# Kernel tuning notes

Measured on AMD Instinct MI355X. Metric: run time of the kernel, lower is better.

The kernel has to match this reference:

```python
import jax, jax.numpy as jnp
import numpy as np

N, E, HID, ED, L, H, D = 65536, 262144, 256, 64, 2, 8, 32
FF = 4 * HID
A_START = 8192  # first action gripper node; nodes [A_START:] are the T*K action nodes


def _ln(x, s, b, eps=1e-5):
    mu = jnp.mean(x, -1, keepdims=True)
    var = jnp.var(x, -1, keepdims=True)
    return (x - mu) * jax.lax.rsqrt(var + eps) * s + b


def _gnn_forward(x, edge_attr, edge_index, Wq, Wk, Wv, WeK, WeV, Wo,
                 ln1_s, ln1_b, ffn_w1, ffn_b1, ffn_w2, ffn_b2, ln2_s, ln2_b):
    # Hetero graph transformer over the single ('gripper','action','gripper') relation:
    # per-layer edge-indexed gather -> multi-head attention with edge features ->
    # segment softmax over incoming edges -> scatter-aggregate -> residual/LN/FFN.
    n = x.shape[0]
    e = edge_attr.shape[0]
    src, dst = edge_index[0], edge_index[1]
    inv_sqrt_d = np.float32(1.0 / np.sqrt(D))
    for l in range(Wq.shape[0]):
        q = (x @ Wq[l]).reshape(n, H, D)
        k = (x @ Wk[l]).reshape(n, H, D)
        v = (x @ Wv[l]).reshape(n, H, D)
        kj = k[src] + (edge_attr @ WeK[l]).reshape(e, H, D)  # [E,H,D] gathered keys + edge bias
        vj = v[src] + (edge_attr @ WeV[l]).reshape(e, H, D)
        score = jnp.einsum('ehd,ehd->eh', q[dst], kj) * inv_sqrt_d  # [E,H]
        smax = jax.ops.segment_max(score, dst, num_segments=n)
        p = jnp.exp(score - smax[dst])
        denom = jax.ops.segment_sum(p, dst, num_segments=n)
        alpha = p / denom[dst]  # segment softmax over incoming edges
        agg = jax.ops.segment_sum((alpha[..., None] * vj).reshape(e, H * D), dst, num_segments=n)
        x = _ln(x + agg @ Wo[l], ln1_s[l], ln1_b[l])
        hid = jax.nn.gelu(x @ ffn_w1[l] + ffn_b1[l], approximate=False) @ ffn_w2[l] + ffn_b2[l]
        x = _ln(x + hid, ln2_s[l], ln2_b[l])
    return x


def setup_inputs() -> dict:
    key = jax.random.key(0)
    ks = iter(jax.random.split(key, 16))
    w = lambda shape: jax.random.normal(next(ks), shape, jnp.float32) * 0.05
    return {
        "all_gripper_feats": jax.random.normal(next(ks), (N, HID), jnp.float32),
        "edge_attr": jax.random.normal(next(ks), (E, ED), jnp.float32),
        "Wq": w((L, HID, H * D)), "Wk": w((L, HID, H * D)), "Wv": w((L, HID, H * D)),
        "WeK": w((L, ED, H * D)), "WeV": w((L, ED, H * D)), "Wo": w((L, H * D, HID)),
        "ln1_s": jnp.ones((L, HID), jnp.float32), "ln1_b": jnp.zeros((L, HID), jnp.float32),
        "ffn_w1": w((L, HID, FF)), "ffn_b1": jnp.zeros((L, FF), jnp.float32),
        "ffn_w2": w((L, FF, HID)), "ffn_b2": jnp.zeros((L, HID), jnp.float32),
        "ln2_s": jnp.ones((L, HID), jnp.float32), "ln2_b": jnp.zeros((L, HID), jnp.float32),
        "head_w1": w((HID, HID)), "head_b1": jnp.zeros((HID,), jnp.float32),
        "head_w2": w((HID, 7)), "head_b2": jnp.zeros((7,), jnp.float32),
        "edge_index": jax.random.randint(next(ks), (2, E), 0, N),
        "action_start": A_START,
    }


def reference(all_gripper_feats, edge_attr, Wq, Wk, Wv, WeK, WeV, Wo,
              ln1_s, ln1_b, ffn_w1, ffn_b1, ffn_w2, ffn_b2, ln2_s, ln2_b,
              head_w1, head_b1, head_w2, head_b2, edge_index, action_start):
    x = _gnn_forward(all_gripper_feats, edge_attr, edge_index, Wq, Wk, Wv, WeK, WeV, Wo,
                     ln1_s, ln1_b, ffn_w1, ffn_b1, ffn_w2, ffn_b2, ln2_s, ln2_b)
    a = x[action_start:]  # action gripper nodes (T*K, hidden)
    return jax.nn.gelu(a @ head_w1 + head_b1, approximate=False) @ head_w2 + head_b2  # (T*K, 7)
```

## Files before the change

kernel.cpp:

```cpp
#include <hip/hip_runtime.h>
#include <hip/hip_bf16.h>
#include <math.h>

#define NN     65536
#define NE     262144
#define HIDN   256
#define EDIM   64
#define NHEAD  8
#define FFN    1024
#define ASTART 8192
#define NACT   (NN - ASTART)
#define NCH    32768
#define NCHP   (NCH + 128)
#define NCHUNK (NE / NCH)
#define DPC    (NN / NCHUNK)
#define RCH    32768

typedef __attribute__((ext_vector_type(8))) short short8;
typedef __attribute__((ext_vector_type(4))) short short4v;
typedef __attribute__((ext_vector_type(4))) float float4v;
typedef __hip_bfloat16 bf16;

__device__ __forceinline__ float b2f(short s) {
    union { unsigned u; float f; } c;
    c.u = ((unsigned)(unsigned short)s) << 16;
    return c.f;
}
__device__ __forceinline__ short f2b(float f) {
    __hip_bfloat16 h = __float2bfloat16(f);
    return *reinterpret_cast<short*>(&h);
}
__device__ __forceinline__ float gelu_fast(float v) {
    const float x  = v * 0.70710678118654752f;
    const float ax = fabsf(x);
    const float t  = __builtin_amdgcn_rcpf(1.0f + 0.3275911f * ax);
    const float y  = t * (0.254829592f + t * (-0.284496736f + t * (1.421413741f +
                     t * (-1.453152027f + t * 1.061405429f))));
    const float e  = __expf(-x * x);
    float erf = 1.0f - y * e;
    erf = copysignf(erf, x);
    return 0.5f * v * (1.0f + erf);
}
__device__ __forceinline__ void gload16(const void* g, void* l) {
    __builtin_amdgcn_global_load_lds(
        (const __attribute__((address_space(1))) void*)(uintptr_t)g,
        (__attribute__((address_space(3))) void*)(unsigned)(uintptr_t)l,
        16, 0, 0);
}

__global__ void convert_kernel(const float* __restrict__ src,
                               bf16* __restrict__ dst, int n) {
    int i = blockIdx.x * 256 + threadIdx.x;
    if (i < n) dst[i] = __float2bfloat16(src[i]);
}
__global__ void convert4_kernel(const float* __restrict__ src,
                                bf16* __restrict__ dst, int n4) {
    int i = blockIdx.x * 256 + threadIdx.x;
    if (i >= n4) return;
    float4v f = *(const float4v*)(src + (size_t)i * 4);
    short4v o;
    #pragma unroll
    for (int j = 0; j < 4; ++j) o[j] = f2b(f[j]);
    *(short4v*)((short*)dst + (size_t)i * 4) = o;
}

__global__ void gather_kernel(const float* __restrict__ src,
                              const int* __restrict__ perm,
                              bf16* __restrict__ dst) {
    int i = blockIdx.x * 256 + threadIdx.x;
    if (i >= NE * 16) return;
    const int p = i >> 4, j = i & 15;
    const float4v f = *(const float4v*)(src + (size_t)perm[p] * EDIM + j * 4);
    short4v o;
    #pragma unroll
    for (int k = 0; k < 4; ++k) o[k] = f2b(f[k]);
    *(short4v*)((short*)dst + (size_t)p * EDIM + j * 4) = o;
}

__global__ void transpose_kernel(const float* __restrict__ src,
                                 bf16* __restrict__ dst, int R, int Cc) {
    int idx = blockIdx.x * 256 + threadIdx.x;
    if (idx >= R * Cc) return;
    int r = idx / Cc, c = idx - r * Cc;
    dst[(size_t)c * R + r] = __float2bfloat16(src[idx]);
}

__global__ void hist_kernel(const int* __restrict__ dstI, int* __restrict__ cnt) {
    int i = blockIdx.x * 256 + threadIdx.x;
    if (i < NE) atomicAdd(&cnt[dstI[i]], 1);
}
__global__ void scan1_kernel(const int* __restrict__ cnt, int* __restrict__ rp,
                             int* __restrict__ bsum) {
    __shared__ int s[256];
    int t = threadIdx.x, i = blockIdx.x * 256 + t;
    int v = cnt[i]; s[t] = v; __syncthreads();
    for (int off = 1; off < 256; off <<= 1) {
        int x = (t >= off) ? s[t - off] : 0; __syncthreads();
        s[t] += x; __syncthreads();
    }
    rp[i] = s[t] - v;
    if (t == 255) bsum[blockIdx.x] = s[255];
}
__global__ void scan2_kernel(int* __restrict__ bsum) {
    __shared__ int s[256];
    int t = threadIdx.x; int v = bsum[t]; s[t] = v; __syncthreads();
    for (int off = 1; off < 256; off <<= 1) {
        int x = (t >= off) ? s[t - off] : 0; __syncthreads();
        s[t] += x; __syncthreads();
    }
    bsum[t] = s[t] - v;
}
__global__ void scan3_kernel(int* __restrict__ rp, const int* __restrict__ bsum,
                             int* __restrict__ cursor) {
    int i = blockIdx.x * 256 + threadIdx.x;
    int v = rp[i] + bsum[i >> 8];
    rp[i] = v; cursor[i] = v;
    if (i == 0) rp[NN] = NE;
}
__global__ void scatter_kernel(const int* __restrict__ srcI, const int* __restrict__ dstI,
                               int* __restrict__ cursor, int* __restrict__ perm,
                               int* __restrict__ src_s, int* __restrict__ dst_s) {
    int e = blockIdx.x * 256 + threadIdx.x;
    if (e >= NE) return;
    int d = dstI[e];
    int pos = atomicAdd(&cursor[d], 1);
    perm[pos] = e; src_s[pos] = srcI[e]; dst_s[pos] = d;
}

template<int AMODE, bool DO_GELU>
__global__ __launch_bounds__(256) void gemm_kernel(
    const void* __restrict__ A,
    const bf16* __restrict__ BT,
    const bf16* __restrict__ bias,
    bf16* __restrict__ C,
    int M, int Nn, int K,
    const int* __restrict__ perm, int permN)
{
    __shared__ __align__(16) short Ls[4][128 * 32];

    const int gx   = gridDim.x;
    const int nwg  = gx * gridDim.y;
    const int orig = blockIdx.y * gx + blockIdx.x;
    const int q8   = nwg >> 3, r8 = nwg & 7;
    const int xcd  = orig & 7, rk = orig >> 3;
    const int nid  = (xcd < r8 ? xcd * (q8 + 1) : r8 * (q8 + 1) + (xcd - r8) * q8) + rk;
    const int by   = nid / gx;
    const int bx   = nid - by * gx;

    const int t    = threadIdx.x;
    const int wave = t >> 6;
    const int lane = t & 63;
    const int l15  = lane & 15;
    const int quad = lane >> 4;
    const int wm   = (wave & 1) * 64;
    const int wn   = (wave >> 1) * 64;
    const int bm   = by * 128;
    const int bn   = bx * 128;
    const int srow = t >> 2;
    const int sw   = srow & 3;
    const int scolB = ((t & 3) ^ sw) * 8;
    const int scolA = (t & 3) * 8;

    const short* Ab = (const short*)A  + (size_t)(bm + srow) * K + scolB;
    const short* Bb = (const short*)BT + (size_t)(bn + srow) * K + scolB;
    const float* Af0 = nullptr;
    const float* Af1 = nullptr;
    if (AMODE == 1) {
        Af0 = (const float*)A + (size_t)(bm + srow) * K + scolA;
        Af1 = Af0 + (size_t)64 * K;
    } else if (AMODE == 2) {
        int i0 = bm + srow;       if (i0 >= permN) i0 = permN - 1;
        int i1 = bm + 64 + srow;  if (i1 >= permN) i1 = permN - 1;
        const int pr0 = perm[i0];
        const int pr1 = perm[i1];
        Af0 = (const float*)A + (size_t)pr0 * K + scolA;
        Af1 = (const float*)A + (size_t)pr1 * K + scolA;
    }
    const int offW  = wave * 1024;
    const int offTs = (t * 16) ^ (sw << 4);
    const int qs16  = (quad ^ (l15 & 3)) * 16;

    float4v acc[4][4];
    #pragma unroll
    for (int i = 0; i < 4; ++i)
        #pragma unroll
        for (int j = 0; j < 4; ++j) acc[i][j] = (float4v){0.f, 0.f, 0.f, 0.f};

    const int nt = K >> 5;

    auto STAGE = [&](int b, int k0) {
        char* lA = (char*)Ls[b];
        char* lB = (char*)Ls[2 + b];
        if (AMODE == 0) {
            gload16(Ab + k0,                  lA + offW);
            gload16(Ab + (size_t)64 * K + k0, lA + 4096 + offW);
        } else {
            #pragma unroll
            for (int i = 0; i < 2; ++i) {
                const float* s = (i ? Af1 : Af0) + k0;
                float4v f0 = *(const float4v*)s;
                float4v f1 = *(const float4v*)(s + 4);
                short8 w;
                #pragma unroll
                for (int j = 0; j < 4; ++j) { w[j] = f2b(f0[j]); w[4 + j] = f2b(f1[j]); }
                *(short8*)(lA + i * 4096 + offTs) = w;
            }
        }
        gload16(Bb + k0,                  lB + offW);
        gload16(Bb + (size_t)64 * K + k0, lB + 4096 + offW);
    };

    STAGE(0, 0);
    __syncthreads();

    for (int kt = 0; kt < nt; ++kt) {
        const int cur = kt & 1;
        if (kt + 1 < nt) STAGE(cur ^ 1, (kt + 1) * 32);

        const char* lA = (const char*)Ls[cur];
        const char* lB = (const char*)Ls[2 + cur];
        short8 afr[4], bfr[4];
        #pragma unroll
        for (int i = 0; i < 4; ++i)
            afr[i] = *(const short8*)(lA + (wm + i * 16 + l15) * 64 + qs16);
        #pragma unroll
        for (int j = 0; j < 4; ++j)
            bfr[j] = *(const short8*)(lB + (wn + j * 16 + l15) * 64 + qs16);
        #pragma unroll
        for (int i = 0; i < 4; ++i)
            #pragma unroll
            for (int j = 0; j < 4; ++j)
                acc[i][j] = __builtin_amdgcn_mfma_f32_16x16x32_bf16(afr[i], bfr[j], acc[i][j], 0, 0, 0);
        __syncthreads();
    }

    short* Ct = (short*)Ls;
    #pragma unroll
    for (int j = 0; j < 4; ++j) {
        const int col  = wn + j * 16 + l15;
        const int pc   = col ^ (quad << 4);
        const float bv = bias ? b2f(((const short*)bias)[bn + col]) : 0.0f;
        #pragma unroll
        for (int i = 0; i < 4; ++i) {
            const int row0 = wm + i * 16 + quad * 4;
            #pragma unroll
            for (int r = 0; r < 4; ++r) {
                float v = acc[i][j][r] + bv;
                if (DO_GELU) v = gelu_fast(v);
                Ct[(row0 + r) * 128 + pc] = f2b(v);
            }
        }
    }
    __syncthreads();
    #pragma unroll
    for (int it = 0; it < 8; ++it) {
        const int row = wave * 32 + it + ((lane >> 4) << 3);
        const int cs  = (lane & 15) * 8;
        const int pcs = cs ^ (((row >> 2) & 3) << 4);
        short8 w = *(const short8*)&Ct[row * 128 + pcs];
        *(short8*)((short*)C + (size_t)(bm + row) * Nn + bn + cs) = w;
    }
}

__global__ __launch_bounds__(256) void score_kernel(
    const bf16* __restrict__ q, const bf16* __restrict__ k,
    const bf16* __restrict__ eK,
    const int* __restrict__ src_s, const int* __restrict__ dst_s,
    short* __restrict__ pbuf, int e0, int qkstride)
{
    const int p = e0 + blockIdx.x * 4 + (threadIdx.x >> 6);
    const int lane = threadIdx.x & 63;
    const int s = src_s[p], d = dst_s[p];
    const int off = lane * 4;

    const short4v qv = *(const short4v*)((const short*)q  + (size_t)d * qkstride + off);
    const short4v kv = *(const short4v*)((const short*)k  + (size_t)s * qkstride + off);
    const short4v ev = *(const short4v*)((const short*)eK + (size_t)(p - e0) * HIDN + off);
    float x = 0.f;
    #pragma unroll
    for (int j = 0; j < 4; ++j) x += b2f(qv[j]) * (b2f(kv[j]) + b2f(ev[j]));
    x += __shfl_xor(x, 1);
    x += __shfl_xor(x, 2);
    x += __shfl_xor(x, 4);
    if ((lane & 7) == 0) {
        const float sc = fminf(fmaxf(x * 0.17677669529663689f, -30.f), 30.f);
        pbuf[(size_t)p * NHEAD + (lane >> 3)] = f2b(expf(sc));
    }
}

__global__ __launch_bounds__(256) void agg_kernel(
    const short* __restrict__ pbuf, const bf16* __restrict__ v,
    const bf16* __restrict__ eV,
    const int* __restrict__ src_s, const int* __restrict__ rp,
    float* __restrict__ agg, int e0, int e1x, int dlo)
{
    const int d = dlo + blockIdx.x * 4 + (threadIdx.x >> 6);
    const int lane = threadIdx.x & 63;
    const int es = rp[d], ee = rp[d + 1];
    if (es < e0 || es >= e1x) return;
    const int h = lane >> 3, off = lane * 4;

    float a0 = 0.f, a1 = 0.f, a2 = 0.f, a3 = 0.f;
    if (es < ee) {
        float den = 0.f;
        for (int p = es; p < ee; ++p) den += b2f(pbuf[(size_t)p * NHEAD + h]);
        const float rden = 1.0f / den;
        for (int p = es; p < ee; ++p) {
            const float al = b2f(pbuf[(size_t)p * NHEAD + h]) * rden;
            const int s = src_s[p];
            const short4v vv = *(const short4v*)((const short*)v  + (size_t)s * HIDN + off);
            const short4v ev = *(const short4v*)((const short*)eV + (size_t)(p - e0) * HIDN + off);
            a0 += al * (b2f(vv[0]) + b2f(ev[0]));
            a1 += al * (b2f(vv[1]) + b2f(ev[1]));
            a2 += al * (b2f(vv[2]) + b2f(ev[2]));
            a3 += al * (b2f(vv[3]) + b2f(ev[3]));
        }
    }
    *(float4v*)(agg + (size_t)d * HIDN + off) = (float4v){a0, a1, a2, a3};
}

__global__ __launch_bounds__(256) void ln_kernel(
    bf16* __restrict__ x, const bf16* __restrict__ t,
    const bf16* __restrict__ sc, const bf16* __restrict__ bi, int r0)
{
    const int row = r0 + blockIdx.x * 4 + (threadIdx.x >> 6);
    const int lane = threadIdx.x & 63;
    const size_t base = (size_t)row * HIDN + lane * 4;
    const size_t tbase = (size_t)(row - r0) * HIDN + lane * 4;
    const short4v xv = *(const short4v*)((const short*)x + base);
    const short4v tv = *(const short4v*)((const short*)t + tbase);
    float v[4];
    #pragma unroll
    for (int j = 0; j < 4; ++j) v[j] = b2f(xv[j]) + b2f(tv[j]);
    float sum = v[0] + v[1] + v[2] + v[3];
    float ssq = v[0]*v[0] + v[1]*v[1] + v[2]*v[2] + v[3]*v[3];
    #pragma unroll
    for (int m = 1; m < 64; m <<= 1) { sum += __shfl_xor(sum, m); ssq += __shfl_xor(ssq, m); }
    const float mean = sum * (1.0f / 256.0f);
    const float var  = fmaxf(ssq * (1.0f / 256.0f) - mean * mean, 0.0f);
    const float rstd = rsqrtf(var + 1e-5f);
    const short4v sv = *(const short4v*)((const short*)sc + lane * 4);
    const short4v bv = *(const short4v*)((const short*)bi + lane * 4);
    short4v out;
    #pragma unroll
    for (int j = 0; j < 4; ++j)
        out[j] = f2b((v[j] - mean) * rstd * b2f(sv[j]) + b2f(bv[j]));
    *(short4v*)((short*)x + base) = out;
}

__global__ __launch_bounds__(256) void head2_kernel(
    const bf16* __restrict__ h1, const bf16* __restrict__ w2T,
    const bf16* __restrict__ b2, float* __restrict__ out)
{
    const int row = blockIdx.x * 4 + (threadIdx.x >> 6);
    const int lane = threadIdx.x & 63;
    const int off = lane * 4;
    const short4v hv = *(const short4v*)((const short*)h1 + (size_t)row * HIDN + off);
    float hf[4];
    #pragma unroll
    for (int j = 0; j < 4; ++j) hf[j] = b2f(hv[j]);
    float acc[7];
    #pragma unroll
    for (int jc = 0; jc < 7; ++jc) {
        const short4v wv = *(const short4v*)((const short*)w2T + jc * HIDN + off);
        float a = hf[0]*b2f(wv[0]) + hf[1]*b2f(wv[1]) + hf[2]*b2f(wv[2]) + hf[3]*b2f(wv[3]);
        #pragma unroll
        for (int m = 1; m < 64; m <<= 1) a += __shfl_xor(a, m);
        acc[jc] = a;
    }
    if (lane < 7) {
        float r = lane == 0 ? acc[0] : lane == 1 ? acc[1] : lane == 2 ? acc[2] :
                  lane == 3 ? acc[3] : lane == 4 ? acc[4] : lane == 5 ? acc[5] : acc[6];
        out[(size_t)row * 7 + lane] = r + b2f(((const short*)b2)[lane]);
    }
}

extern "C" void kernel_launch(void* const* d_in, const int* in_sizes, int n_in,
                              void* d_out, int out_size, void* d_ws, size_t ws_size,
                              hipStream_t stream)
{
    const float* xin   = (const float*)d_in[0];
    const float* eattr = (const float*)d_in[1];
    const float* Wq    = (const float*)d_in[2];
    const float* Wk    = (const float*)d_in[3];
    const float* Wv    = (const float*)d_in[4];
    const float* WeK   = (const float*)d_in[5];
    const float* WeV   = (const float*)d_in[6];
    const float* Wo    = (const float*)d_in[7];
    const float* ln1s  = (const float*)d_in[8];
    const float* ln1b  = (const float*)d_in[9];
    const float* fw1   = (const float*)d_in[10];
    const float* fb1   = (const float*)d_in[11];
    const float* fw2   = (const float*)d_in[12];
    const float* fb2   = (const float*)d_in[13];
    const float* ln2s  = (const float*)d_in[14];
    const float* ln2b  = (const float*)d_in[15];
    const float* hw1   = (const float*)d_in[16];
    const float* hb1   = (const float*)d_in[17];
    const float* hw2   = (const float*)d_in[18];
    const float* hb2   = (const float*)d_in[19];
    const int*  eidx   = (const int*)d_in[20];
    const int*  srcI   = eidx;
    const int*  dstI   = eidx + NE;

    char* base = (char*)d_ws;
    size_t off = 0;
    auto carve = [&](size_t bytes) -> char* {
        char* p = base + off;
        off += (bytes + 255) & ~(size_t)255;
        return p;
    };
    bf16*  x_b    = (bf16*) carve((size_t)NN * HIDN * 2);
    bf16*  qk_b   = (bf16*) carve((size_t)NN * 2 * HIDN * 2);
    bf16*  v_b    = (bf16*) carve((size_t)NN * HIDN * 2);
    bf16*  echunk = (bf16*) carve((size_t)NCHP * HIDN * 2);
    short* pbuf   = (short*)carve((size_t)NE * NHEAD * 2);
    int*   perm   = (int*)  carve((size_t)NE * 4);
    int*   src_s  = (int*)  carve((size_t)NE * 4);
    int*   dst_s  = (int*)  carve((size_t)NE * 4);
    int*   rowp   = (int*)  carve((size_t)(NN + 1) * 4);
    bf16*  WqkT   = (bf16*) carve((size_t)2 * HIDN * HIDN * 2);
    bf16*  WvT    = (bf16*) carve((size_t)HIDN * HIDN * 2);
    bf16*  WoT    = (bf16*) carve((size_t)HIDN * HIDN * 2);
    bf16*  WeKT   = (bf16*) carve((size_t)HIDN * EDIM * 2);
    bf16*  WeVT   = (bf16*) carve((size_t)HIDN * EDIM * 2);
    bf16*  W1T    = (bf16*) carve((size_t)FFN * HIDN * 2);
    bf16*  W2T    = (bf16*) carve((size_t)HIDN * FFN * 2);
    bf16*  HW1T   = (bf16*) carve((size_t)HIDN * HIDN * 2);
    bf16*  HW2T   = (bf16*) carve((size_t)8 * HIDN * 2);
    bf16*  c_ln1s = (bf16*) carve((size_t)2 * HIDN * 2);
    bf16*  c_ln1b = (bf16*) carve((size_t)2 * HIDN * 2);
    bf16*  c_ln2s = (bf16*) carve((size_t)2 * HIDN * 2);
    bf16*  c_ln2b = (bf16*) carve((size_t)2 * HIDN * 2);
    bf16*  c_fb1  = (bf16*) carve((size_t)2 * FFN * 2);
    bf16*  c_fb2  = (bf16*) carve((size_t)2 * HIDN * 2);
    bf16*  c_hb1  = (bf16*) carve((size_t)HIDN * 2);
    bf16*  c_hb2  = (bf16*) carve((size_t)16 * 2);
    const size_t off_mand = off;
    bf16*  eattr_s = (bf16*) carve((size_t)(NE + 128) * EDIM * 2);
    const bool eg = (off <= ws_size);
    if (off_mand > ws_size) return;

    int* cnt    = (int*)echunk;
    int* cursor = cnt + NN;
    int* bsum   = cursor + NN;
    float* agg    = (float*)qk_b;
    bf16*  tmp_b  = v_b;
    bf16*  hid    = qk_b;
    bf16*  ffnout = v_b;

    const int TB = 256;
    #define GRID1(n) dim3(((n) + TB - 1) / TB)

    convert4_kernel<<<GRID1(NN * HIDN / 4), TB, 0, stream>>>(xin, x_b, NN * HIDN / 4);
    convert_kernel<<<GRID1(2 * HIDN), TB, 0, stream>>>(ln1s, c_ln1s, 2 * HIDN);
    convert_kernel<<<GRID1(2 * HIDN), TB, 0, stream>>>(ln1b, c_ln1b, 2 * HIDN);
    convert_kernel<<<GRID1(2 * HIDN), TB, 0, stream>>>(ln2s, c_ln2s, 2 * HIDN);
    convert_kernel<<<GRID1(2 * HIDN), TB, 0, stream>>>(ln2b, c_ln2b, 2 * HIDN);
    convert_kernel<<<GRID1(2 * FFN), TB, 0, stream>>>(fb1, c_fb1, 2 * FFN);
    convert_kernel<<<GRID1(2 * HIDN), TB, 0, stream>>>(fb2, c_fb2, 2 * HIDN);
    convert_kernel<<<GRID1(HIDN), TB, 0, stream>>>(hb1, c_hb1, HIDN);
    convert_kernel<<<1, TB, 0, stream>>>(hb2, c_hb2, 7);
    transpose_kernel<<<GRID1(HIDN * HIDN), TB, 0, stream>>>(hw1, HW1T, HIDN, HIDN);
    transpose_kernel<<<GRID1(HIDN * 7), TB, 0, stream>>>(hw2, HW2T, HIDN, 7);

    hipMemsetAsync(cnt, 0, (size_t)NN * 4, stream);
    hist_kernel<<<GRID1(NE), TB, 0, stream>>>(dstI, cnt);
    scan1_kernel<<<NN / 256, 256, 0, stream>>>(cnt, rowp, bsum);
    scan2_kernel<<<1, 256, 0, stream>>>(bsum);
    scan3_kernel<<<NN / 256, 256, 0, stream>>>(rowp, bsum, cursor);
    scatter_kernel<<<GRID1(NE), TB, 0, stream>>>(srcI, dstI, cursor, perm, src_s, dst_s);
    if (eg) gather_kernel<<<GRID1(NE * 16), TB, 0, stream>>>(eattr, perm, eattr_s);

    for (int l = 0; l < 2; ++l) {
        transpose_kernel<<<GRID1(HIDN * HIDN), TB, 0, stream>>>(Wq + (size_t)l*HIDN*HIDN, WqkT, HIDN, HIDN);
        transpose_kernel<<<GRID1(HIDN * HIDN), TB, 0, stream>>>(Wk + (size_t)l*HIDN*HIDN, WqkT + (size_t)HIDN*HIDN, HIDN, HIDN);
        transpose_kernel<<<GRID1(HIDN * HIDN), TB, 0, stream>>>(Wv + (size_t)l*HIDN*HIDN, WvT, HIDN, HIDN);
        transpose_kernel<<<GRID1(EDIM * HIDN), TB, 0, stream>>>(WeK + (size_t)l*EDIM*HIDN, WeKT, EDIM, HIDN);
        transpose_kernel<<<GRID1(EDIM * HIDN), TB, 0, stream>>>(WeV + (size_t)l*EDIM*HIDN, WeVT, EDIM, HIDN);
        transpose_kernel<<<GRID1(HIDN * HIDN), TB, 0, stream>>>(Wo + (size_t)l*HIDN*HIDN, WoT, HIDN, HIDN);
        transpose_kernel<<<GRID1(HIDN * FFN),  TB, 0, stream>>>(fw1 + (size_t)l*HIDN*FFN, W1T, HIDN, FFN);
        transpose_kernel<<<GRID1(FFN * HIDN),  TB, 0, stream>>>(fw2 + (size_t)l*FFN*HIDN, W2T, FFN, HIDN);

        gemm_kernel<0, false><<<dim3((2*HIDN)/128, NN/128), TB, 0, stream>>>(x_b, WqkT, nullptr, qk_b, NN, 2*HIDN, HIDN, nullptr, 0);
        gemm_kernel<0, false><<<dim3(HIDN/128, NN/128), TB, 0, stream>>>(x_b, WvT, nullptr, v_b, NN, HIDN, HIDN, nullptr, 0);

        for (int c = 0; c < NCHUNK; ++c) {
            if (eg)
                gemm_kernel<0, false><<<dim3(HIDN/128, NCH/128), TB, 0, stream>>>(
                    eattr_s + (size_t)c * NCH * EDIM, WeKT, nullptr, echunk, NCH, HIDN, EDIM, nullptr, 0);
            else
                gemm_kernel<2, false><<<dim3(HIDN/128, NCH/128), TB, 0, stream>>>(
                    eattr, WeKT, nullptr, echunk, NCH, HIDN, EDIM, perm + (size_t)c * NCH, NE - c * NCH);
            score_kernel<<<NCH / 4, TB, 0, stream>>>(qk_b, qk_b + HIDN, echunk, src_s, dst_s, pbuf, c * NCH, 2 * HIDN);
        }

        for (int c = 0; c < NCHUNK; ++c) {
            if (eg)
                gemm_kernel<0, false><<<dim3(HIDN/128, NCHP/128), TB, 0, stream>>>(
                    eattr_s + (size_t)c * NCH * EDIM, WeVT, nullptr, echunk, NCHP, HIDN, EDIM, nullptr, 0);
            else
                gemm_kernel<2, false><<<dim3(HIDN/128, NCHP/128), TB, 0, stream>>>(
                    eattr, WeVT, nullptr, echunk, NCHP, HIDN, EDIM, perm + (size_t)c * NCH, NE - c * NCH);
            const int dlo = (c == 0) ? 0 : (c - 1) * DPC;
            const int dhi = (c == NCHUNK - 1) ? NN : (c + 2) * DPC;
            const int e1x = (c == NCHUNK - 1) ? NE + 1 : (c + 1) * NCH;
            agg_kernel<<<(dhi - dlo) / 4, TB, 0, stream>>>(
                pbuf, v_b, echunk, src_s, rowp, agg, c * NCH, e1x, dlo);
        }

        gemm_kernel<1, false><<<dim3(HIDN/128, NN/128), TB, 0, stream>>>(agg, WoT, nullptr, tmp_b, NN, HIDN, HIDN, nullptr, 0);
        ln_kernel<<<NN / 4, TB, 0, stream>>>(x_b, tmp_b, c_ln1s + (size_t)l * HIDN, c_ln1b + (size_t)l * HIDN, 0);

        for (int r0 = 0; r0 < NN; r0 += RCH) {
            gemm_kernel<0, true ><<<dim3(FFN/128, RCH/128), TB, 0, stream>>>(
                x_b + (size_t)r0 * HIDN, W1T, c_fb1 + (size_t)l * FFN, hid, RCH, FFN, HIDN, nullptr, 0);
            gemm_kernel<0, false><<<dim3(HIDN/128, RCH/128), TB, 0, stream>>>(
                hid, W2T, c_fb2 + (size_t)l * HIDN, ffnout, RCH, HIDN, FFN, nullptr, 0);
            ln_kernel<<<RCH / 4, TB, 0, stream>>>(x_b, ffnout, c_ln2s + (size_t)l * HIDN, c_ln2b + (size_t)l * HIDN, r0);
        }
    }

    gemm_kernel<0, true><<<dim3(HIDN/128, NACT/128), TB, 0, stream>>>(
        x_b + (size_t)ASTART * HIDN, HW1T, c_hb1, hid, NACT, HIDN, HIDN, nullptr, 0);
    head2_kernel<<<NACT / 4, TB, 0, stream>>>(hid, HW2T, c_hb2, (float*)d_out);
}
```

Before: 1.497 ms.

## Use three-stage LDS ring with vmcnt-based waits for direct-load GEMM path

For the AMODE 0 GEMM path (direct global-to-LDS loads), the double-buffered loop is replaced with a three-slot ring buffer that prefetches two k-tiles ahead. Each iteration uses an explicit s_waitcnt on vmcnt and one raw s_barrier instead of a full __syncthreads, so more global loads stay in flight while MFMAs run. This costs more LDS per workgroup, which can lower occupancy, and depends on the vmcnt(4) count matching the four loads issued per stage. The gather path (AMODE 1) keeps the old double-buffered loop.

```diff
diff --git a/kernel.cpp b/kernel.cpp
--- a/kernel.cpp
+++ b/kernel.cpp
@@ -136,7 +136,8 @@
     int M, int Nn, int K,
     const int* __restrict__ perm, int permN)
 {
-    __shared__ __align__(16) short Ls[4][128 * 32];
+    constexpr int RING = (AMODE == 0) ? 3 : 2;
+    __shared__ __align__(16) short Ls[2 * RING][128 * 32];
 
     const int gx   = gridDim.x;
     const int nwg  = gx * gridDim.y;
@@ -190,7 +191,7 @@
 
     auto STAGE = [&](int b, int k0) {
         char* lA = (char*)Ls[b];
-        char* lB = (char*)Ls[2 + b];
+        char* lB = (char*)Ls[RING + b];
         if (AMODE == 0) {
             gload16(Ab + k0,                  lA + offW);
             gload16(Ab + (size_t)64 * K + k0, lA + 4096 + offW);
@@ -210,15 +211,9 @@
         gload16(Bb + (size_t)64 * K + k0, lB + 4096 + offW);
     };
 
-    STAGE(0, 0);
-    __syncthreads();
-
-    for (int kt = 0; kt < nt; ++kt) {
-        const int cur = kt & 1;
-        if (kt + 1 < nt) STAGE(cur ^ 1, (kt + 1) * 32);
-
-        const char* lA = (const char*)Ls[cur];
-        const char* lB = (const char*)Ls[2 + cur];
+    auto COMPUTE = [&](int b) {
+        const char* lA = (const char*)Ls[b];
+        const char* lB = (const char*)Ls[RING + b];
         short8 afr[4], bfr[4];
         #pragma unroll
         for (int i = 0; i < 4; ++i)
@@ -231,7 +226,39 @@
             #pragma unroll
             for (int j = 0; j < 4; ++j)
                 acc[i][j] = __builtin_amdgcn_mfma_f32_16x16x32_bf16(afr[i], bfr[j], acc[i][j], 0, 0, 0);
+    };
+
+    if (AMODE == 0) {
+        STAGE(0, 0);
+        STAGE(1, 32);
+        for (int kt = 0; kt < nt - 2; ++kt) {
+            asm volatile("s_waitcnt vmcnt(4) lgkmcnt(0)" ::: "memory");
+            __builtin_amdgcn_sched_barrier(0);
+            __builtin_amdgcn_s_barrier();
+            __builtin_amdgcn_sched_barrier(0);
+            STAGE((kt + 2) % 3, (kt + 2) * 32);
+            COMPUTE(kt % 3);
+        }
+        asm volatile("s_waitcnt vmcnt(4) lgkmcnt(0)" ::: "memory");
+        __builtin_amdgcn_sched_barrier(0);
+        __builtin_amdgcn_s_barrier();
+        __builtin_amdgcn_sched_barrier(0);
+        COMPUTE((nt - 2) % 3);
+        asm volatile("s_waitcnt vmcnt(0) lgkmcnt(0)" ::: "memory");
+        __builtin_amdgcn_sched_barrier(0);
+        __builtin_amdgcn_s_barrier();
+        __builtin_amdgcn_sched_barrier(0);
+        COMPUTE((nt - 1) % 3);
         __syncthreads();
+    } else {
+        STAGE(0, 0);
+        __syncthreads();
+        for (int kt = 0; kt < nt; ++kt) {
+            const int cur = kt & 1;
+            if (kt + 1 < nt) STAGE(cur ^ 1, (kt + 1) * 32);
+            COMPUTE(cur);
+            __syncthreads();
+        }
     }
 
     short* Ct = (short*)Ls;
```

After: 1.504 ms. No clear change (+0.5%).
